# Kernel tuning notes

Hardware: AMD Instinct MI355X
Metric: run time of the kernel (lower is better)

Reference implementation:

```python
import jax, jax.numpy as jnp
import numpy as np

DIM = 768
NUM_HEADS = 12
HEAD_DIM = DIM // NUM_HEADS
SCALE = HEAD_DIM ** -0.5


def setup_inputs() -> dict:
    key = jax.random.key(0)
    ks = jax.random.split(key, 6)
    B, Lq, Lkv = 8, 1024, 1024
    return {
        "q": jax.random.normal(ks[0], (B, Lq, DIM), dtype=jnp.float32),
        "kv": jax.random.normal(ks[1], (B, Lkv, DIM), dtype=jnp.float32),
        "attn_pos": jax.random.normal(ks[2], (1, NUM_HEADS, Lq, Lkv), dtype=jnp.float32),
        "Wq": jax.random.normal(ks[3], (DIM, DIM), dtype=jnp.float32) * (DIM ** -0.5),
        "Wkv": jax.random.normal(ks[4], (2 * DIM, DIM), dtype=jnp.float32) * (DIM ** -0.5),
        "Wproj": jax.random.normal(ks[5], (DIM, DIM), dtype=jnp.float32) * (DIM ** -0.5),
        "bproj": jnp.zeros((DIM,), dtype=jnp.float32),
    }


def reference(q, kv, attn_pos, Wq, Wkv, Wproj, bproj):
    B, Lq, C = q.shape
    Lkv = kv.shape[1]
    H, D = NUM_HEADS, HEAD_DIM
    # q/kv projections (torch Linear: x @ W.T); attn_pos_encoding_only path
    qh = (q @ Wq.T).reshape(B, Lq, H, D).transpose(0, 2, 1, 3)        # (B,H,Lq,D)
    kvp = (kv @ Wkv.T).reshape(B, Lkv, 2, H, D).transpose(2, 0, 3, 1, 4)
    k, v = kvp[0], kvp[1]                                             # (B,H,Lkv,D)
    # scaled dot-product attention with additive positional bias
    attn = jnp.einsum('bhqd,bhkd->bhqk', qh, k) * SCALE + attn_pos    # (B,H,Lq,Lkv)
    attn = jax.nn.softmax(attn, axis=-1)
    x = jnp.einsum('bhqk,bhkd->bhqd', attn, v)                        # (B,H,Lq,D)
    x = x.transpose(0, 2, 1, 3).reshape(B, Lq, C)
    return x @ Wproj.T + bproj
```

## Files before the change

### kernel.cpp

```cpp
#include <hip/hip_runtime.h>

#define DIM 768
#define NHEADS 12
#define HDIM 64
#define BATCH 8
#define LQ 1024
#define LKV 1024
#define ATTN_SCALE 0.125f
#define LOG2E 1.4426950408889634f
#define C1_SL2E 0.18033688011112042f

typedef __bf16 bf16;
typedef __bf16 bf16x4 __attribute__((ext_vector_type(4)));
typedef __bf16 bf16x8 __attribute__((ext_vector_type(8)));
typedef short s16x4 __attribute__((ext_vector_type(4)));
typedef float f32x4 __attribute__((ext_vector_type(4)));

union B4 { bf16x4 h; s16x4 s; };

static __device__ __forceinline__ f32x4 mfma_k32(bf16x8 a, bf16x8 b, f32x4 c) {
    return __builtin_amdgcn_mfma_f32_16x16x32_bf16(a, b, c, 0, 0, 0);
}
static __device__ __forceinline__ f32x4 mfma_k16(s16x4 a, s16x4 b, f32x4 c) {
    return __builtin_amdgcn_mfma_f32_16x16x16bf16_1k(a, b, c, 0, 0, 0);
}

static __device__ __forceinline__ void async16(const bf16* g, bf16* l) {
    __builtin_amdgcn_global_load_lds(
        (const __attribute__((address_space(1))) unsigned int*)g,
        (__attribute__((address_space(3))) unsigned int*)l, 16, 0, 0);
}
static __device__ __forceinline__ void drain_vmem() {
    __asm__ volatile("s_waitcnt vmcnt(0)" ::: "memory");
}
#define WAIT_VMCNT(N) __asm__ volatile("s_waitcnt vmcnt(" #N ")" ::: "memory")
static __device__ __forceinline__ void code_fence() {
    __asm__ volatile("" ::: "memory");
}

#define NQ4 (BATCH * LQ * DIM / 4)
#define NW4 (DIM * DIM / 4)
__global__ void cvt_all(const float4* __restrict__ q, const float4* __restrict__ kv,
                        const float4* __restrict__ Wq, const float4* __restrict__ Wkv,
                        const float4* __restrict__ Wp,
                        bf16x4* __restrict__ qb, bf16x4* __restrict__ kvb,
                        bf16x4* __restrict__ wall, bf16x4* __restrict__ wpb) {
    int i = blockIdx.x * 256 + threadIdx.x;
    const float4* src; bf16x4* dst; int j;
    if (i < NQ4)                { src = q;   dst = qb;        j = i; }
    else if (i < 2 * NQ4)       { src = kv;  dst = kvb;       j = i - NQ4; }
    else if (i < 2 * NQ4 + NW4) { src = Wq;  dst = wall;      j = i - 2 * NQ4; }
    else if (i < 2 * NQ4 + 3 * NW4) { src = Wkv; dst = wall + NW4; j = i - 2 * NQ4 - NW4; }
    else if (i < 2 * NQ4 + 4 * NW4) { src = Wp;  dst = wpb;   j = i - 2 * NQ4 - 3 * NW4; }
    else return;
    float4 v = src[j];
    bf16x4 o;
    o[0] = (bf16)v.x; o[1] = (bf16)v.y; o[2] = (bf16)v.z; o[3] = (bf16)v.w;
    dst[j] = o;
}

__global__ __launch_bounds__(256) void proj_gemm(
    const bf16* __restrict__ qb, const bf16* __restrict__ kvb,
    const bf16* __restrict__ W,
    bf16* __restrict__ Qp, bf16* __restrict__ Kp, bf16* __restrict__ Vt)
{
    __shared__ bf16 As[128 * 32];
    __shared__ bf16 Bs[128 * 32];
    const int tid  = threadIdx.x;
    const int lane = tid & 63;
    const int w    = tid >> 6;
    const int wm = (w >> 1) * 64;
    const int wn = (w & 1) * 64;
    const int m0 = blockIdx.x * 128;
    const int n0 = blockIdx.y * 128;
    const int K = DIM;
    const int lq = lane & 15;
    const int quad = lane >> 4;

    const bf16* A = (n0 < DIM) ? qb : kvb;
    const int isV = (n0 >= 2 * DIM);

    const int rl = lane >> 2;
    const int ck = (lane & 3) * 8;
    const bf16* gA = A + (size_t)(m0 + w * 32 + rl) * K + ck;
    const bf16* gB = W + (size_t)(n0 + w * 32 + rl) * K + ck;
    bf16* lA = &As[w * 1024];
    bf16* lB = &Bs[w * 1024];

    f32x4 acc[4][4] = {};

    for (int k0 = 0; k0 < K; k0 += 32) {
        async16(gA + k0,                  lA);
        async16(gA + (size_t)16 * K + k0, lA + 512);
        async16(gB + k0,                  lB);
        async16(gB + (size_t)16 * K + k0, lB + 512);
        drain_vmem();
        __syncthreads();

        bf16x8 a[4], b[4];
        #pragma unroll
        for (int i = 0; i < 4; i++)
            a[i] = *(const bf16x8*)&As[(wm + i * 16 + lq) * 32 + quad * 8];
        #pragma unroll
        for (int j = 0; j < 4; j++)
            b[j] = *(const bf16x8*)&Bs[(wn + j * 16 + lq) * 32 + quad * 8];
        if (isV) {
            #pragma unroll
            for (int i = 0; i < 4; i++)
                #pragma unroll
                for (int j = 0; j < 4; j++)
                    acc[i][j] = mfma_k32(a[i], b[j], acc[i][j]);
        } else {
            #pragma unroll
            for (int i = 0; i < 4; i++)
                #pragma unroll
                for (int j = 0; j < 4; j++)
                    acc[i][j] = mfma_k32(b[j], a[i], acc[i][j]);
        }
        __syncthreads();
    }

    if (isV) {
        const int n0v = n0 - 2 * DIM;
        #pragma unroll
        for (int i = 0; i < 4; i++) {
            const int base_m = m0 + wm + i * 16;
            const int b_idx = base_m >> 10;
            const int kvl = (base_m & 1023) + quad * 4;
            #pragma unroll
            for (int j = 0; j < 4; j++) {
                const int nl = n0v + wn + j * 16 + lq;
                const int h = nl >> 6;
                const int d = nl & 63;
                B4 pk;
                #pragma unroll
                for (int r = 0; r < 4; r++) pk.h[r] = (bf16)acc[i][j][r];
                *(s16x4*)&Vt[(((size_t)b_idx * NHEADS + h) * HDIM + d) * LKV + kvl] = pk.s;
            }
        }
    } else {
        bf16* Cb = (n0 < DIM) ? Qp : Kp;
        const float cs = (n0 < DIM) ? C1_SL2E : 1.0f;
        const int nb = (n0 < DIM) ? n0 : n0 - DIM;
        #pragma unroll
        for (int i = 0; i < 4; i++) {
            const size_t row = m0 + wm + i * 16 + lq;
            #pragma unroll
            for (int j = 0; j < 4; j++) {
                const int col = nb + wn + j * 16 + quad * 4;
                B4 pk;
                #pragma unroll
                for (int r = 0; r < 4; r++) pk.h[r] = (bf16)(acc[i][j][r] * cs);
                *(s16x4*)&Cb[row * DIM + col] = pk.s;
            }
        }
    }
}

__global__ __launch_bounds__(256) void out_gemm(
    const bf16* __restrict__ A, const bf16* __restrict__ B,
    float* __restrict__ Cp, const float* __restrict__ bias, int M, int N, int K)
{
    __shared__ bf16 As[64 * 32];
    __shared__ bf16 Bs[128 * 32];
    const int tid  = threadIdx.x;
    const int lane = tid & 63;
    const int w    = tid >> 6;
    const int wm = (w >> 1) * 32;
    const int wn = (w & 1) * 64;
    const int m0 = blockIdx.x * 64;
    const int n0 = blockIdx.y * 128;
    const int lq = lane & 15;
    const int quad = lane >> 4;

    const int rl = lane >> 2;
    const int ck = (lane & 3) * 8;
    const bf16* gA = A + (size_t)(m0 + w * 16 + rl) * K + ck;
    const bf16* gB = B + (size_t)(n0 + w * 32 + rl) * K + ck;
    bf16* lA = &As[w * 512];
    bf16* lB = &Bs[w * 1024];

    f32x4 acc[2][4] = {};

    for (int k0 = 0; k0 < K; k0 += 32) {
        async16(gA + k0,                  lA);
        async16(gB + k0,                  lB);
        async16(gB + (size_t)16 * K + k0, lB + 512);
        drain_vmem();
        __syncthreads();

        bf16x8 a[2], b[4];
        #pragma unroll
        for (int i = 0; i < 2; i++)
            a[i] = *(const bf16x8*)&As[(wm + i * 16 + lq) * 32 + quad * 8];
        #pragma unroll
        for (int j = 0; j < 4; j++)
            b[j] = *(const bf16x8*)&Bs[(wn + j * 16 + lq) * 32 + quad * 8];
        #pragma unroll
        for (int i = 0; i < 2; i++)
            #pragma unroll
            for (int j = 0; j < 4; j++)
                acc[i][j] = mfma_k32(b[j], a[i], acc[i][j]);
        __syncthreads();
    }

    #pragma unroll
    for (int i = 0; i < 2; i++) {
        const size_t row = m0 + wm + i * 16 + lq;
        #pragma unroll
        for (int j = 0; j < 4; j++) {
            const int col = n0 + wn + j * 16 + quad * 4;
            float4 bj = *(const float4*)&bias[col];
            float4 o;
            o.x = acc[i][j][0] + bj.x; o.y = acc[i][j][1] + bj.y;
            o.z = acc[i][j][2] + bj.z; o.w = acc[i][j][3] + bj.w;
            *(float4*)&Cp[row * N + col] = o;
        }
    }
}

__global__ __launch_bounds__(256) void attn_kernel(
    const bf16* __restrict__ Qb,
    const bf16* __restrict__ Kb,
    const bf16* __restrict__ Vt,
    const float* __restrict__ pos,
    bf16* __restrict__ O)
{
    __shared__ bf16 Ks[2][64 * 64];
    __shared__ bf16 Vs[2][64 * 64];

    const int i  = blockIdx.x;
    const int g  = (i & 7) * 24 + (i >> 6);
    const int b  = (i >> 3) & 7;
    const int h  = g >> 4;
    const int q0 = (g & 15) * 64;
    const int bh = b * NHEADS + h;
    const int t = threadIdx.x;
    const int lane = t & 63;
    const int w = t >> 6;
    const int lq = lane & 15;
    const int quad = lane >> 4;

    const bf16* qg = Qb + (size_t)(b * LQ + q0 + w * 16 + lq) * DIM + h * HDIM + quad * 8;
    bf16x8 qa0 = *(const bf16x8*)(qg);
    bf16x8 qa1 = *(const bf16x8*)(qg + 32);

    const int srow  = t >> 3;
    const int chunk = t & 7;
    const int sw    = (chunk ^ (srow & 7)) * 8;
    const bf16* Kg = Kb + (size_t)(b * LKV + srow) * DIM + h * HDIM + sw;
    const bf16* Vg = Vt + (size_t)(bh * HDIM + srow) * LKV + sw;

#define STAGE(kv0, bufi) do {                                                                 \
    async16(Kg + (size_t)(kv0) * DIM,        &Ks[bufi][srow * 64 + chunk * 8]);               \
    async16(Kg + (size_t)((kv0) + 32) * DIM, &Ks[bufi][(srow + 32) * 64 + chunk * 8]);        \
    async16(Vg + (kv0),                      &Vs[bufi][srow * 64 + chunk * 8]);               \
    async16(Vg + (size_t)32 * LKV + (kv0),   &Vs[bufi][(srow + 32) * 64 + chunk * 8]);        \
} while (0)

#define NT (LKV / 64)

    const float4* pos4 = (const float4*)(pos + ((size_t)h * LQ + q0 + w * 16 + lq) * LKV);

    float l_r = 0.f;
    f32x4 o_acc[4] = {};

    STAGE(0, 0);
    float4 pA0 = pos4[quad],      pA1 = pos4[4 + quad];
    float4 pA2 = pos4[8 + quad],  pA3 = pos4[12 + quad];
    float4 pB0 = pos4[16 + quad], pB1 = pos4[20 + quad];
    float4 pB2 = pos4[24 + quad], pB3 = pos4[28 + quad];
    WAIT_VMCNT(8);
    __builtin_amdgcn_s_barrier();
    code_fence();

#define SMB(KB, P) do {                                          \
    float p0 = exp2f(fmaf((P).x, LOG2E, sc[KB][0]));             \
    float p1 = exp2f(fmaf((P).y, LOG2E, sc[KB][1]));             \
    float p2 = exp2f(fmaf((P).z, LOG2E, sc[KB][2]));             \
    float p3 = exp2f(fmaf((P).w, LOG2E, sc[KB][3]));             \
    l_r += (p0 + p1) + (p2 + p3);                                \
    pfrag[KB].h[0] = (bf16)p0; pfrag[KB].h[1] = (bf16)p1;        \
    pfrag[KB].h[2] = (bf16)p2; pfrag[KB].h[3] = (bf16)p3;        \
} while (0)

#define BODY(IT, BUF, P0, P1, P2, P3) do {                                                     \
    if ((IT) + 1 < NT) STAGE(((IT) + 1) * 64, (BUF) ^ 1);                                      \
    f32x4 sc[4];                                                                               \
    __builtin_amdgcn_s_setprio(1);                                                             \
    _Pragma("unroll")                                                                          \
    for (int kb = 0; kb < 4; kb++) {                                                           \
        const int krow = kb * 16 + lq;                                                         \
        bf16x8 ak0 = *(const bf16x8*)&Ks[BUF][krow * 64 + ((quad) ^ (lq & 7)) * 8];            \
        bf16x8 ak1 = *(const bf16x8*)&Ks[BUF][krow * 64 + ((4 + quad) ^ (lq & 7)) * 8];        \
        sc[kb] = mfma_k32(ak0, qa0, (f32x4){0.f, 0.f, 0.f, 0.f});                              \
        sc[kb] = mfma_k32(ak1, qa1, sc[kb]);                                                   \
    }                                                                                          \
    __builtin_amdgcn_s_setprio(0);                                                             \
    B4 pfrag[4];                                                                               \
    SMB(0, P0); SMB(1, P1); SMB(2, P2); SMB(3, P3);                                            \
    if ((IT) + 2 < NT) {                                                                       \
        const int pb = ((IT) + 2) * 16 + quad;                                                 \
        P0 = pos4[pb]; P1 = pos4[pb + 4]; P2 = pos4[pb + 8]; P3 = pos4[pb + 12];               \
    }                                                                                          \
    __builtin_amdgcn_s_setprio(1);                                                             \
    _Pragma("unroll")                                                                          \
    for (int db = 0; db < 4; db++) {                                                           \
        const int vrow = db * 16 + lq;                                                         \
        _Pragma("unroll")                                                                      \
        for (int kb = 0; kb < 4; kb++) {                                                       \
            s16x4 va = *(const s16x4*)&Vs[BUF][vrow * 64                                       \
                          + (((kb * 2 + (quad >> 1)) ^ (lq & 7)) * 8) + (quad & 1) * 4];       \
            o_acc[db] = mfma_k16(va, pfrag[kb].s, o_acc[db]);                                  \
        }                                                                                      \
    }                                                                                          \
    __builtin_amdgcn_s_setprio(0);                                                             \
    if ((IT) + 1 < NT) {                                                                       \
        WAIT_VMCNT(4);                             \
        __builtin_amdgcn_s_barrier();                           \
        code_fence();                                  \
    }                                                                                          \
} while (0)

    for (int it2 = 0; it2 < NT; it2 += 2) {
        BODY(it2,     0, pA0, pA1, pA2, pA3);
        BODY(it2 + 1, 1, pB0, pB1, pB2, pB3);
    }
#undef BODY
#undef SMB
#undef STAGE

    l_r += __shfl_xor(l_r, 16);
    l_r += __shfl_xor(l_r, 32);
    float inv = 1.f / l_r;
    const size_t orow = (size_t)(b * LQ + q0 + w * 16 + lq) * DIM + h * HDIM;
    #pragma unroll
    for (int dblk = 0; dblk < 4; dblk++) {
        B4 ob;
        #pragma unroll
        for (int r = 0; r < 4; r++) ob.h[r] = (bf16)(o_acc[dblk][r] * inv);
        *(s16x4*)&O[orow + dblk * 16 + quad * 4] = ob.s;
    }
}

extern "C" void kernel_launch(void* const* d_in, const int* in_sizes, int n_in,
                              void* d_out, int out_size, void* d_ws, size_t ws_size,
                              hipStream_t stream) {
    const float* q     = (const float*)d_in[0];
    const float* kv    = (const float*)d_in[1];
    const float* pos   = (const float*)d_in[2];
    const float* Wq    = (const float*)d_in[3];
    const float* Wkv   = (const float*)d_in[4];
    const float* Wproj = (const float*)d_in[5];
    const float* bproj = (const float*)d_in[6];
    float* out = (float*)d_out;

    char* ws = (char*)d_ws;
    size_t off = 0;
    auto alloc = [&](size_t bytes) -> void* {
        void* p = ws + off;
        off += (bytes + 255) & ~(size_t)255;
        return p;
    };

    const int M = BATCH * LQ;
    bf16* qb   = (bf16*)alloc((size_t)M * DIM * 2);
    bf16* kvb  = (bf16*)alloc((size_t)M * DIM * 2);
    bf16* wall = (bf16*)alloc((size_t)3 * DIM * DIM * 2);
    bf16* wpb  = (bf16*)alloc((size_t)DIM * DIM * 2);
    bf16* Qp   = (bf16*)alloc((size_t)M * DIM * 2);
    bf16* Kp   = (bf16*)alloc((size_t)M * DIM * 2);
    bf16* Vt   = (bf16*)alloc((size_t)BATCH * NHEADS * HDIM * LKV * 2);
    bf16* Ob   = (bf16*)alloc((size_t)M * DIM * 2);

    {
        int total = 2 * NQ4 + 4 * NW4;
        cvt_all<<<(total + 255) / 256, 256, 0, stream>>>(
            (const float4*)q, (const float4*)kv, (const float4*)Wq,
            (const float4*)Wkv, (const float4*)Wproj,
            (bf16x4*)qb, (bf16x4*)kvb, (bf16x4*)wall, (bf16x4*)wpb);
    }

    proj_gemm<<<dim3(M / 128, (3 * DIM) / 128), 256, 0, stream>>>(qb, kvb, wall, Qp, Kp, Vt);
    attn_kernel<<<dim3((LQ / 64) * NHEADS * BATCH), 256, 0, stream>>>(Qp, Kp, Vt, pos, Ob);
    out_gemm<<<dim3(M / 64, DIM / 128), 256, 0, stream>>>(Ob, wpb, out, bproj, M, DIM, DIM);
}
```

Baseline: 285.3 us.

## Interleave QK MFMAs with softmax and compute row sums via ones-MFMA

Restructures the attention inner loop so each QK score block's exp is computed while the next block's MFMA runs, instead of finishing all QK MFMAs before any softmax. The row-sum of probabilities is now accumulated with an extra MFMA against a ones vector, which drops the scalar adds and the cross-lane shuffles at the end. Positional-bias prefetch shrinks from two iterations ahead to one, which halves the registers held for it but leaves less time to hide the load latency. The row sum is now formed from bf16-rounded probabilities, a small change in numerics.

```diff
diff --git a/kernel.cpp b/kernel.cpp
--- a/kernel.cpp
+++ b/kernel.cpp
@@ -262,48 +262,53 @@
 
     const float4* pos4 = (const float4*)(pos + ((size_t)h * LQ + q0 + w * 16 + lq) * LKV);
 
-    float l_r = 0.f;
+    B4 onesb;
+    onesb.s = (s16x4){0x3F80, 0x3F80, 0x3F80, 0x3F80};
+
     f32x4 o_acc[4] = {};
+    f32x4 o_l = {};
 
     STAGE(0, 0);
     float4 pA0 = pos4[quad],      pA1 = pos4[4 + quad];
     float4 pA2 = pos4[8 + quad],  pA3 = pos4[12 + quad];
-    float4 pB0 = pos4[16 + quad], pB1 = pos4[20 + quad];
-    float4 pB2 = pos4[24 + quad], pB3 = pos4[28 + quad];
-    WAIT_VMCNT(8);
+    WAIT_VMCNT(4);
     __builtin_amdgcn_s_barrier();
     code_fence();
 
-#define SMB(KB, P) do {                                          \
-    float p0 = exp2f(fmaf((P).x, LOG2E, sc[KB][0]));             \
-    float p1 = exp2f(fmaf((P).y, LOG2E, sc[KB][1]));             \
-    float p2 = exp2f(fmaf((P).z, LOG2E, sc[KB][2]));             \
-    float p3 = exp2f(fmaf((P).w, LOG2E, sc[KB][3]));             \
-    l_r += (p0 + p1) + (p2 + p3);                                \
-    pfrag[KB].h[0] = (bf16)p0; pfrag[KB].h[1] = (bf16)p1;        \
-    pfrag[KB].h[2] = (bf16)p2; pfrag[KB].h[3] = (bf16)p3;        \
+#define QK(BUF, KB, S) do {                                                                   \
+    const int krow = (KB) * 16 + lq;                                                          \
+    bf16x8 ak0 = *(const bf16x8*)&Ks[BUF][krow * 64 + ((quad) ^ (lq & 7)) * 8];               \
+    bf16x8 ak1 = *(const bf16x8*)&Ks[BUF][krow * 64 + ((4 + quad) ^ (lq & 7)) * 8];           \
+    S = mfma_k32(ak0, qa0, (f32x4){0.f, 0.f, 0.f, 0.f});                                      \
+    S = mfma_k32(ak1, qa1, S);                                                                \
 } while (0)
 
-#define BODY(IT, BUF, P0, P1, P2, P3) do {                                                     \
+#define SMB(S, P, PF) do {                                       \
+    float p0 = exp2f(fmaf((P).x, LOG2E, (S)[0]));                \
+    float p1 = exp2f(fmaf((P).y, LOG2E, (S)[1]));                \
+    float p2 = exp2f(fmaf((P).z, LOG2E, (S)[2]));                \
+    float p3 = exp2f(fmaf((P).w, LOG2E, (S)[3]));                \
+    (PF).h[0] = (bf16)p0; (PF).h[1] = (bf16)p1;                  \
+    (PF).h[2] = (bf16)p2; (PF).h[3] = (bf16)p3;                  \
+} while (0)
+
+#define BODY(IT, BUF) do {                                                                     \
     if ((IT) + 1 < NT) STAGE(((IT) + 1) * 64, (BUF) ^ 1);                                      \
-    f32x4 sc[4];                                                                               \
+    const int pbn = ((IT) + 1) * 16 + quad;                                                    \
+    B4 pf[4];                                                                                  \
+    f32x4 s0, s1, s2, s3;                                                                      \
     __builtin_amdgcn_s_setprio(1);                                                             \
+    QK(BUF, 0, s0);                                                                            \
+    QK(BUF, 1, s1);                                                                            \
+    SMB(s0, pA0, pf[0]); if ((IT) + 1 < NT) pA0 = pos4[pbn];                                   \
+    QK(BUF, 2, s2);                                                                            \
+    SMB(s1, pA1, pf[1]); if ((IT) + 1 < NT) pA1 = pos4[pbn + 4];                               \
+    QK(BUF, 3, s3);                                                                            \
+    SMB(s2, pA2, pf[2]); if ((IT) + 1 < NT) pA2 = pos4[pbn + 8];                               \
+    SMB(s3, pA3, pf[3]); if ((IT) + 1 < NT) pA3 = pos4[pbn + 12];                              \
     _Pragma("unroll")                                                                          \
-    for (int kb = 0; kb < 4; kb++) {                                                           \
-        const int krow = kb * 16 + lq;                                                         \
-        bf16x8 ak0 = *(const bf16x8*)&Ks[BUF][krow * 64 + ((quad) ^ (lq & 7)) * 8];            \
-        bf16x8 ak1 = *(const bf16x8*)&Ks[BUF][krow * 64 + ((4 + quad) ^ (lq & 7)) * 8];        \
-        sc[kb] = mfma_k32(ak0, qa0, (f32x4){0.f, 0.f, 0.f, 0.f});                              \
-        sc[kb] = mfma_k32(ak1, qa1, sc[kb]);                                                   \
-    }                                                                                          \
-    __builtin_amdgcn_s_setprio(0);                                                             \
-    B4 pfrag[4];                                                                               \
-    SMB(0, P0); SMB(1, P1); SMB(2, P2); SMB(3, P3);                                            \
-    if ((IT) + 2 < NT) {                                                                       \
-        const int pb = ((IT) + 2) * 16 + quad;                                                 \
-        P0 = pos4[pb]; P1 = pos4[pb + 4]; P2 = pos4[pb + 8]; P3 = pos4[pb + 12];               \
-    }                                                                                          \
-    __builtin_amdgcn_s_setprio(1);                                                             \
+    for (int kb = 0; kb < 4; kb++)                                                             \
+        o_l = mfma_k16(onesb.s, pf[kb].s, o_l);                                                \
     _Pragma("unroll")                                                                          \
     for (int db = 0; db < 4; db++) {                                                           \
         const int vrow = db * 16 + lq;                                                         \
@@ -311,7 +316,7 @@
         for (int kb = 0; kb < 4; kb++) {                                                       \
             s16x4 va = *(const s16x4*)&Vs[BUF][vrow * 64                                       \
                           + (((kb * 2 + (quad >> 1)) ^ (lq & 7)) * 8) + (quad & 1) * 4];       \
-            o_acc[db] = mfma_k16(va, pfrag[kb].s, o_acc[db]);                                  \
+            o_acc[db] = mfma_k16(va, pf[kb].s, o_acc[db]);                                     \
         }                                                                                      \
     }                                                                                          \
     __builtin_amdgcn_s_setprio(0);                                                             \
@@ -323,16 +328,15 @@
 } while (0)
 
     for (int it2 = 0; it2 < NT; it2 += 2) {
-        BODY(it2,     0, pA0, pA1, pA2, pA3);
-        BODY(it2 + 1, 1, pB0, pB1, pB2, pB3);
+        BODY(it2,     0);
+        BODY(it2 + 1, 1);
     }
 #undef BODY
 #undef SMB
+#undef QK
 #undef STAGE
 
-    l_r += __shfl_xor(l_r, 16);
-    l_r += __shfl_xor(l_r, 32);
-    float inv = 1.f / l_r;
+    float inv = 1.f / o_l[0];
     const size_t orow = (size_t)(b * LQ + q0 + w * 16 + lq) * DIM + h * HDIM;
     #pragma unroll
     for (int dblk = 0; dblk < 4; dblk++) {
```

Result: no change. 288.0 us (+0.9%).
